# Kernel optimization log

Hardware: AMD Instinct MI355X
Metric: run time of the kernel (lower is better)

Reference implementation:

```python
import jax, jax.numpy as jnp
import numpy as np

EPS = 1e-6

def _rms_norm(x, w):
    # normalize over last dim (head_dim)
    var = jnp.mean(jnp.square(x), axis=-1, keepdims=True)
    return x * jax.lax.rsqrt(var + EPS) * w

def _rotate_half(x):
    half = x.shape[-1] // 2
    first, second = x[..., :half], x[..., half:]
    return jnp.concatenate([-second, first], axis=-1)

def _apply_rope(x, cos, sin):
    # x: [B,H,S,D]; cos/sin: [B,S,D] -> broadcast over heads
    return x * cos[:, None] + _rotate_half(x) * sin[:, None]

def setup_inputs() -> dict:
    key = jax.random.key(0)
    ks = jax.random.split(key, 10)
    B, Sq, Sk, Dm, H = 2, 2048, 2048, 2048, 16
    hd = Dm // H
    scale = 1.0 / np.sqrt(Dm)
    return {
        "x": jax.random.normal(ks[0], (B, Sq, Dm), jnp.float32),
        "context": jax.random.normal(ks[1], (B, Sk, Dm), jnp.float32),
        "cos_q": jax.random.uniform(ks[2], (B, Sq, hd), jnp.float32),
        "sin_q": jax.random.uniform(ks[3], (B, Sq, hd), jnp.float32),
        "cos_k": jax.random.uniform(ks[4], (B, Sk, hd), jnp.float32),
        "sin_k": jax.random.uniform(ks[5], (B, Sk, hd), jnp.float32),
        "Wq": jax.random.normal(ks[6], (Dm, Dm), jnp.float32) * scale,
        "Wk": jax.random.normal(ks[7], (Dm, Dm), jnp.float32) * scale,
        "Wv": jax.random.normal(ks[8], (Dm, Dm), jnp.float32) * scale,
        "Wo": jax.random.normal(ks[9], (Dm, Dm), jnp.float32) * scale,
        "q_norm_w": jnp.ones((hd,), jnp.float32),
        "k_norm_w": jnp.ones((hd,), jnp.float32),
    }

def reference(x, context, cos_q, sin_q, cos_k, sin_k, Wq, Wk, Wv, Wo, q_norm_w, k_norm_w):
    B, Sq, Dm = x.shape
    hd = q_norm_w.shape[0]
    H = Dm // hd
    # projections (torch Linear: y = x @ W.T), reshape to [B,H,S,D]
    q = (x @ Wq.T).reshape(B, Sq, H, hd).transpose(0, 2, 1, 3)
    k = (context @ Wk.T).reshape(B, -1, H, hd).transpose(0, 2, 1, 3)
    v = (context @ Wv.T).reshape(B, -1, H, hd).transpose(0, 2, 1, 3)
    # per-head QK RMSNorm
    q = _rms_norm(q, q_norm_w)
    k = _rms_norm(k, k_norm_w)
    # RoPE
    q = _apply_rope(q, cos_q, sin_q)
    k = _apply_rope(k, cos_k, sin_k)
    # SDPA, scale = 1/sqrt(head_dim)
    scale = 1.0 / np.sqrt(hd).astype(np.float32)
    scores = jnp.einsum('bhqd,bhkd->bhqk', q, k) * scale
    attn = jax.nn.softmax(scores, axis=-1)
    y = jnp.einsum('bhqk,bhkd->bhqd', attn, v)
    y = y.transpose(0, 2, 1, 3).reshape(B, Sq, Dm)
    return y @ Wo.T
```

## Files before the change

kernel.cpp:

```cpp
#include <hip/hip_runtime.h>


typedef __attribute__((ext_vector_type(8))) short bf16x8;
typedef __attribute__((ext_vector_type(4))) float f32x4;

#define AS1(p) ((__attribute__((address_space(1))) void*)(p))
#define AS3(p) ((__attribute__((address_space(3))) void*)(p))

__device__ __forceinline__ unsigned short f2bf(float f) {
  unsigned int u = __float_as_uint(f);
  u += 0x7fffu + ((u >> 16) & 1u);
  return (unsigned short)(u >> 16);
}
__device__ __forceinline__ float bf2f(unsigned short u) {
  return __uint_as_float(((unsigned int)u) << 16);
}

constexpr int B_ = 2, S_ = 2048, DM = 2048, H_ = 16, HD = 128;
constexpr int M_ = B_ * S_;

__global__ __launch_bounds__(256) void castbf(const float* __restrict__ X,
                                              unsigned short* __restrict__ Y, int n4) {
  int i = blockIdx.x * 256 + threadIdx.x;
  if (i >= n4) return;
  float4 v = ((const float4*)X)[i];
  ushort4 u;
  u.x = f2bf(v.x); u.y = f2bf(v.y); u.z = f2bf(v.z); u.w = f2bf(v.w);
  ((ushort4*)Y)[i] = u;
}

__global__ __launch_bounds__(256) void gemm_qkv(const unsigned short* __restrict__ xb,
                                                const unsigned short* __restrict__ cb,
                                                const unsigned short* __restrict__ Wq,
                                                const unsigned short* __restrict__ Wk,
                                                const unsigned short* __restrict__ Wv,
                                                unsigned short* __restrict__ Pq,
                                                unsigned short* __restrict__ Pk,
                                                unsigned short* __restrict__ Pv) {
  __shared__ unsigned short lA[128 * 32];
  __shared__ unsigned short lB[128 * 32];
  const int z = blockIdx.z;
  const unsigned short* A  = (z == 0) ? xb : cb;
  const unsigned short* Bw = (z == 0) ? Wq : (z == 1) ? Wk : Wv;
  unsigned short* C        = (z == 0) ? Pq : (z == 1) ? Pk : Pv;
  const int tid = threadIdx.x, wave = tid >> 6, lane = tid & 63;
  const int quad = lane >> 4, l16 = lane & 15;
  const int m0 = blockIdx.x * 128, n0 = blockIdx.y * 128;
  const int wm = (wave >> 1) * 64, wn = (wave & 1) * 64;
  f32x4 acc[4][4];
#pragma unroll
  for (int i = 0; i < 4; i++)
#pragma unroll
    for (int j = 0; j < 4; j++) acc[i][j] = (f32x4){0.f, 0.f, 0.f, 0.f};

  for (int k0 = 0; k0 < DM; k0 += 32) {
    __syncthreads();
#pragma unroll
    for (int call = 0; call < 2; ++call) {
      int c = wave * 128 + call * 64 + lane;
      int row = c >> 2, s = c & 3;
      int dc = s ^ ((row >> 1) & 3);
      __builtin_amdgcn_global_load_lds(AS1(A + (size_t)(m0 + row) * DM + k0 + dc * 8),
                                       AS3(lA + (wave * 128 + call * 64) * 8), 16, 0, 0);
      __builtin_amdgcn_global_load_lds(AS1(Bw + (size_t)(n0 + row) * DM + k0 + dc * 8),
                                       AS3(lB + (wave * 128 + call * 64) * 8), 16, 0, 0);
    }
    __syncthreads();

    bf16x8 af[4], bfr[4];
#pragma unroll
    for (int i = 0; i < 4; i++) {
      int r = wm + i * 16 + l16;
      af[i] = *(const bf16x8*)(lA + r * 32 + (quad ^ ((r >> 1) & 3)) * 8);
      int cN = wn + i * 16 + l16;
      bfr[i] = *(const bf16x8*)(lB + cN * 32 + (quad ^ ((cN >> 1) & 3)) * 8);
    }
#pragma unroll
    for (int i = 0; i < 4; i++)
#pragma unroll
      for (int j = 0; j < 4; j++)
        acc[i][j] = __builtin_amdgcn_mfma_f32_16x16x32_bf16(af[i], bfr[j], acc[i][j], 0, 0, 0);
  }
#pragma unroll
  for (int i = 0; i < 4; i++)
#pragma unroll
    for (int j = 0; j < 4; j++) {
      unsigned short* cp = C + (size_t)(m0 + wm + i * 16 + quad * 4) * DM + (n0 + wn + j * 16 + l16);
#pragma unroll
      for (int r = 0; r < 4; r++) cp[(size_t)r * DM] = f2bf(acc[i][j][r]);
    }
}

__global__ __launch_bounds__(256) void gemm_bt(const unsigned short* __restrict__ A,
                                               const unsigned short* __restrict__ Bw,
                                               float* __restrict__ C,
                                               int M, int N, int K) {
  __shared__ unsigned short lA[128 * 32];
  __shared__ unsigned short lB[128 * 32];
  const int tid = threadIdx.x, wave = tid >> 6, lane = tid & 63;
  const int quad = lane >> 4, l16 = lane & 15;
  const int m0 = blockIdx.x * 128, n0 = blockIdx.y * 128;
  const int wm = (wave >> 1) * 64, wn = (wave & 1) * 64;
  f32x4 acc[4][4];
#pragma unroll
  for (int i = 0; i < 4; i++)
#pragma unroll
    for (int j = 0; j < 4; j++) acc[i][j] = (f32x4){0.f, 0.f, 0.f, 0.f};

  for (int k0 = 0; k0 < K; k0 += 32) {
    __syncthreads();
#pragma unroll
    for (int call = 0; call < 2; ++call) {
      int c = wave * 128 + call * 64 + lane;
      int row = c >> 2, s = c & 3;
      int dc = s ^ ((row >> 1) & 3);
      __builtin_amdgcn_global_load_lds(AS1(A + (size_t)(m0 + row) * K + k0 + dc * 8),
                                       AS3(lA + (wave * 128 + call * 64) * 8), 16, 0, 0);
      __builtin_amdgcn_global_load_lds(AS1(Bw + (size_t)(n0 + row) * K + k0 + dc * 8),
                                       AS3(lB + (wave * 128 + call * 64) * 8), 16, 0, 0);
    }
    __syncthreads();

    bf16x8 af[4], bfr[4];
#pragma unroll
    for (int i = 0; i < 4; i++) {
      int r = wm + i * 16 + l16;
      af[i] = *(const bf16x8*)(lA + r * 32 + (quad ^ ((r >> 1) & 3)) * 8);
      int cN = wn + i * 16 + l16;
      bfr[i] = *(const bf16x8*)(lB + cN * 32 + (quad ^ ((cN >> 1) & 3)) * 8);
    }
#pragma unroll
    for (int i = 0; i < 4; i++)
#pragma unroll
      for (int j = 0; j < 4; j++)
        acc[i][j] = __builtin_amdgcn_mfma_f32_16x16x32_bf16(af[i], bfr[j], acc[i][j], 0, 0, 0);
  }
#pragma unroll
  for (int i = 0; i < 4; i++)
#pragma unroll
    for (int j = 0; j < 4; j++) {
      float* cp = C + (size_t)(m0 + wm + i * 16 + quad * 4) * N + (n0 + wn + j * 16 + l16);
#pragma unroll
      for (int r = 0; r < 4; r++) cp[(size_t)r * N] = acc[i][j][r];
    }
}

__global__ __launch_bounds__(256) void normrope(const unsigned short* __restrict__ X,
                                                const float* __restrict__ Cs,
                                                const float* __restrict__ Sn,
                                                const float* __restrict__ W,
                                                unsigned short* __restrict__ Out,
                                                float scale) {
  int gw = (blockIdx.x * 256 + threadIdx.x) >> 6;
  int lane = threadIdx.x & 63;
  int h = gw & 15, bs = gw >> 4;
  int s = bs & (S_ - 1), b = bs >> 11;
  const unsigned short* xr = X + (size_t)gw * HD;
  float x0 = bf2f(xr[lane]), x1 = bf2f(xr[lane + 64]);
  float ss = x0 * x0 + x1 * x1;
#pragma unroll
  for (int off = 32; off > 0; off >>= 1) ss += __shfl_xor(ss, off);
  float rr = rsqrtf(ss * (1.0f / 128.0f) + 1e-6f);
  float n0 = x0 * rr * W[lane], n1 = x1 * rr * W[lane + 64];
  const float* cp = Cs + (size_t)bs * HD;
  const float* sp = Sn + (size_t)bs * HD;
  float o0 = (n0 * cp[lane] - n1 * sp[lane]) * scale;
  float o1 = (n1 * cp[lane + 64] + n0 * sp[lane + 64]) * scale;
  unsigned short* orow = Out + (((size_t)(b * H_ + h)) * S_ + s) * HD;
  orow[lane] = f2bf(o0);
  orow[lane + 64] = f2bf(o1);
}

__global__ __launch_bounds__(256) void vtrans(const unsigned short* __restrict__ Vf,
                                              unsigned short* __restrict__ Vt) {
  __shared__ unsigned short tile[128 * 72];
  const int tid = threadIdx.x;
  const int sc = blockIdx.x & 31;
  const int bh = blockIdx.x >> 5;
  const int b = bh >> 4, h = bh & 15;
  const int s0 = sc * 64;
#pragma unroll
  for (int it = 0; it < 4; ++it) {
    int ci = it * 256 + tid;
    int s = ci >> 4, dc = ci & 15;
    bf16x8 v = *(const bf16x8*)(Vf + ((size_t)(b * S_ + s0 + s)) * DM + h * HD + dc * 8);
    unsigned short* tp = tile + (dc * 8) * 72 + s;
#pragma unroll
    for (int e = 0; e < 8; e++) tp[e * 72] = (unsigned short)v[e];
  }
  __syncthreads();
#pragma unroll
  for (int it = 0; it < 4; ++it) {
    int cj = it * 256 + tid;
    int d = cj >> 3, scx = cj & 7;
    bf16x8 vv = *(const bf16x8*)(tile + d * 72 + scx * 8);
    *(bf16x8*)(Vt + ((size_t)bh * HD + d) * S_ + s0 + scx * 8) = vv;
  }
}

__global__ __launch_bounds__(128) void flash(const unsigned short* __restrict__ Q,
                                             const unsigned short* __restrict__ Kt,
                                             const unsigned short* __restrict__ Vt,
                                             unsigned short* __restrict__ Y) {
  __shared__ unsigned short lK[64 * HD];
  __shared__ unsigned short lV[HD * 64];
  __shared__ unsigned short lP[2 * 1024];
  const int tid = threadIdx.x, wave = tid >> 6, lane = tid & 63;
  const int quad = lane >> 4, l16 = lane & 15;
  const int qb = blockIdx.x & 31;
  const int bh = blockIdx.x >> 5;
  const int b = bh >> 4, h = bh & 15;
  const int q0 = qb * 64 + wave * 32;

  bf16x8 aq[2][4];
#pragma unroll
  for (int u = 0; u < 2; u++) {
    const unsigned short* qrow = Q + ((size_t)bh * S_ + q0 + u * 16 + l16) * HD;
#pragma unroll
    for (int t = 0; t < 4; t++) aq[u][t] = *(const bf16x8*)(qrow + t * 32 + quad * 8);
  }
  f32x4 o[2][8];
#pragma unroll
  for (int u = 0; u < 2; u++)
#pragma unroll
    for (int t = 0; t < 8; t++) o[u][t] = (f32x4){0.f, 0.f, 0.f, 0.f};
  float lsum[2][4] = {{0.f, 0.f, 0.f, 0.f}, {0.f, 0.f, 0.f, 0.f}};

  const unsigned short* kbase = Kt + (size_t)bh * S_ * HD;
  const unsigned short* vbase = Vt + (size_t)bh * HD * S_;
  unsigned short* lPw = lP + wave * 1024;
  const int mrow = quad * 4;
  const int xsl = (l16 >> 1) & 3;
  const int xsl7 = (l16 >> 1) & 7;

  for (int k0 = 0; k0 < S_; k0 += 64) {
    __syncthreads();
#pragma unroll
    for (int call = 0; call < 8; ++call) {
      int c = call * 128 + wave * 64 + lane;
      int key = c >> 4, sk = c & 15;
      int dck = sk ^ (key & 15);
      __builtin_amdgcn_global_load_lds(AS1(kbase + (size_t)(k0 + key) * HD + dck * 8),
                                       AS3(lK + (call * 128 + wave * 64) * 8), 16, 0, 0);
      int dv = c >> 3, sv = c & 7;
      int kc = sv ^ ((dv >> 1) & 7);
      __builtin_amdgcn_global_load_lds(AS1(vbase + (size_t)dv * S_ + k0 + kc * 8),
                                       AS3(lV + (call * 128 + wave * 64) * 8), 16, 0, 0);
    }
    __syncthreads();

#pragma unroll
    for (int h2 = 0; h2 < 2; ++h2) {
      f32x4 s0[2] = {(f32x4){0.f, 0.f, 0.f, 0.f}, (f32x4){0.f, 0.f, 0.f, 0.f}};
      f32x4 s1[2] = {(f32x4){0.f, 0.f, 0.f, 0.f}, (f32x4){0.f, 0.f, 0.f, 0.f}};
      {
        const unsigned short* krow0 = lK + (h2 * 32 + l16) * HD;
        const unsigned short* krow1 = krow0 + 16 * HD;
#pragma unroll
        for (int t = 0; t < 4; t++) {
          int dcq = t * 4 + quad;
          bf16x8 kf0 = *(const bf16x8*)(krow0 + (dcq ^ l16) * 8);
          bf16x8 kf1 = *(const bf16x8*)(krow1 + (dcq ^ l16) * 8);
#pragma unroll
          for (int u = 0; u < 2; u++) {
            s0[u] = __builtin_amdgcn_mfma_f32_16x16x32_bf16(aq[u][t], kf0, s0[u], 0, 0, 0);
            s1[u] = __builtin_amdgcn_mfma_f32_16x16x32_bf16(aq[u][t], kf1, s1[u], 0, 0, 0);
          }
        }
      }
#pragma unroll
      for (int u = 0; u < 2; u++) {
        unsigned short* lPu = lPw + u * 512;
#pragma unroll
        for (int r = 0; r < 4; r++) {
          int m = mrow + r;
          int sx = (m >> 1) & 3;
          float p0 = __expf(s0[u][r]);
          float p1 = __expf(s1[u][r]);
          lsum[u][r] += p0 + p1;
          int kc0 = l16 >> 3;
          lPu[m * 32 + ((kc0 ^ sx)) * 8 + (l16 & 7)] = f2bf(p0);
          lPu[m * 32 + (((kc0 + 2) ^ sx)) * 8 + (l16 & 7)] = f2bf(p1);
        }
      }
      bf16x8 pf[2];
#pragma unroll
      for (int u = 0; u < 2; u++)
        pf[u] = *(const bf16x8*)(lPw + u * 512 + l16 * 32 + (quad ^ xsl) * 8);
#pragma unroll
      for (int t = 0; t < 8; t++) {
        bf16x8 vf = *(const bf16x8*)(lV + (t * 16 + l16) * 64 + ((h2 * 4 + quad) ^ xsl7) * 8);
#pragma unroll
        for (int u = 0; u < 2; u++)
          o[u][t] = __builtin_amdgcn_mfma_f32_16x16x32_bf16(pf[u], vf, o[u][t], 0, 0, 0);
      }
    }
  }

#pragma unroll
  for (int off = 1; off < 16; off <<= 1) {
#pragma unroll
    for (int u = 0; u < 2; u++)
#pragma unroll
      for (int r = 0; r < 4; r++) lsum[u][r] += __shfl_xor(lsum[u][r], off);
  }
  float inv[2][4];
#pragma unroll
  for (int u = 0; u < 2; u++)
#pragma unroll
    for (int r = 0; r < 4; r++) inv[u][r] = 1.0f / lsum[u][r];
#pragma unroll
  for (int u = 0; u < 2; u++)
#pragma unroll
    for (int t = 0; t < 8; t++)
#pragma unroll
      for (int r = 0; r < 4; r++) {
        size_t idx = ((size_t)b * S_ + q0 + u * 16 + mrow + r) * DM + h * HD + t * 16 + l16;
        Y[idx] = f2bf(o[u][t][r] * inv[u][r]);
      }
}

extern "C" void kernel_launch(void* const* d_in, const int* in_sizes, int n_in,
                              void* d_out, int out_size, void* d_ws, size_t ws_size,
                              hipStream_t stream) {
  const float* x    = (const float*)d_in[0];
  const float* ctx  = (const float*)d_in[1];
  const float* cosq = (const float*)d_in[2];
  const float* sinq = (const float*)d_in[3];
  const float* cosk = (const float*)d_in[4];
  const float* sink = (const float*)d_in[5];
  const float* Wq   = (const float*)d_in[6];
  const float* Wk   = (const float*)d_in[7];
  const float* Wv   = (const float*)d_in[8];
  const float* Wo   = (const float*)d_in[9];
  const float* qw   = (const float*)d_in[10];
  const float* kw   = (const float*)d_in[11];

  char* ws = (char*)d_ws;
  const size_t ACT2 = (size_t)M_ * DM * 2;
  const size_t W2   = (size_t)DM * DM * 2;
  unsigned short* xb  = (unsigned short*)(ws);
  unsigned short* cb  = (unsigned short*)(ws + ACT2);
  unsigned short* Wqb = (unsigned short*)(ws + 2 * ACT2);
  unsigned short* Wkb = (unsigned short*)(ws + 2 * ACT2 + W2);
  unsigned short* Wvb = (unsigned short*)(ws + 2 * ACT2 + 2 * W2);
  unsigned short* Wob = (unsigned short*)(ws + 2 * ACT2 + 3 * W2);
  unsigned short* Pq  = (unsigned short*)(ws + 2 * ACT2 + 4 * W2);
  unsigned short* Pk  = (unsigned short*)(ws + 3 * ACT2 + 4 * W2);
  unsigned short* Pv  = (unsigned short*)(ws + 4 * ACT2 + 4 * W2);
  unsigned short* qn = xb;
  unsigned short* kn = Wqb;
  unsigned short* vt = cb;
  unsigned short* yb = Pq;

  const float scale = 0.0883883476483184f;

  castbf<<<M_ * DM / 1024, 256, 0, stream>>>(x, xb, M_ * DM / 4);
  castbf<<<M_ * DM / 1024, 256, 0, stream>>>(ctx, cb, M_ * DM / 4);
  castbf<<<DM * DM / 1024, 256, 0, stream>>>(Wq, Wqb, DM * DM / 4);
  castbf<<<DM * DM / 1024, 256, 0, stream>>>(Wk, Wkb, DM * DM / 4);
  castbf<<<DM * DM / 1024, 256, 0, stream>>>(Wv, Wvb, DM * DM / 4);
  castbf<<<DM * DM / 1024, 256, 0, stream>>>(Wo, Wob, DM * DM / 4);

  dim3 gq(M_ / 128, DM / 128, 3);
  gemm_qkv<<<gq, 256, 0, stream>>>(xb, cb, Wqb, Wkb, Wvb, Pq, Pk, Pv);

  normrope<<<M_ * H_ / 4, 256, 0, stream>>>(Pq, cosq, sinq, qw, qn, scale);
  normrope<<<M_ * H_ / 4, 256, 0, stream>>>(Pk, cosk, sink, kw, kn, 1.0f);
  vtrans<<<B_ * H_ * (S_ / 64), 256, 0, stream>>>(Pv, vt);

  flash<<<B_ * H_ * (S_ / 64), 128, 0, stream>>>(qn, kn, vt, yb);

  dim3 gg(M_ / 128, DM / 128);
  gemm_bt<<<gg, 256, 0, stream>>>(yb, Wob, (float*)d_out, M_, DM, DM);

  (void)in_sizes; (void)n_in; (void)out_size; (void)ws_size;
}
```

Measured before the change: 499.2 us.

## Pipeline GEMMs with 4-stage LDS ring, 256x128 tiles, and MFMA priority boosts

```diff
diff --git a/kernel.cpp b/kernel.cpp
--- a/kernel.cpp
+++ b/kernel.cpp
@@ -29,120 +29,113 @@
   ((ushort4*)Y)[i] = u;
 }
 
-__global__ __launch_bounds__(256) void gemm_qkv(const unsigned short* __restrict__ xb,
-                                                const unsigned short* __restrict__ cb,
-                                                const unsigned short* __restrict__ Wq,
-                                                const unsigned short* __restrict__ Wk,
-                                                const unsigned short* __restrict__ Wv,
-                                                unsigned short* __restrict__ Pq,
-                                                unsigned short* __restrict__ Pk,
-                                                unsigned short* __restrict__ Pv) {
-  __shared__ unsigned short lA[128 * 32];
-  __shared__ unsigned short lB[128 * 32];
+template <int BF16OUT>
+__device__ __forceinline__ void gemm_core(const unsigned short* __restrict__ A,
+                                          const unsigned short* __restrict__ Bw,
+                                          void* __restrict__ Cv,
+                                          unsigned short* lA, unsigned short* lB) {
+  const int tid = threadIdx.x, wave = tid >> 6, lane = tid & 63;
+  const int quad = lane >> 4, l16 = lane & 15;
+  const int m0 = blockIdx.x * 256, n0 = blockIdx.y * 128;
+  const int wm = (wave >> 1) * 64, wn = (wave & 1) * 64;
+  constexpr int NT = DM / 32;
+
+  f32x4 acc[4][4];
+#pragma unroll
+  for (int i = 0; i < 4; i++)
+#pragma unroll
+    for (int j = 0; j < 4; j++) acc[i][j] = (f32x4){0.f, 0.f, 0.f, 0.f};
+
+  const int c0 = wave * 64 + lane;
+  const int rA0 = c0 >> 2, dA0 = (c0 & 3) ^ ((rA0 >> 1) & 3);
+  const int c1 = 512 + c0;
+  const int rA1 = c1 >> 2, dA1 = (c1 & 3) ^ ((rA1 >> 1) & 3);
+  const unsigned short* gA0 = A + (size_t)(m0 + rA0) * DM + dA0 * 8;
+  const unsigned short* gA1 = A + (size_t)(m0 + rA1) * DM + dA1 * 8;
+  const unsigned short* gB  = Bw + (size_t)(n0 + rA0) * DM + dA0 * 8;
+  const int wdst = wave * 512;
+
+#define STAGE(T)                                                                         \
+  {                                                                                      \
+    const int b_ = (T) & 3; const int k_ = (T) << 5;                                     \
+    __builtin_amdgcn_global_load_lds(AS1(gA0 + k_), AS3(lA + b_ * 8192 + wdst), 16, 0, 0);\
+    __builtin_amdgcn_global_load_lds(AS1(gA1 + k_), AS3(lA + b_ * 8192 + 4096 + wdst), 16, 0, 0);\
+    __builtin_amdgcn_global_load_lds(AS1(gB + k_),  AS3(lB + b_ * 4096 + wdst), 16, 0, 0);\
+  }
+
+  STAGE(0) STAGE(1) STAGE(2)
+
+  const int xoff = (quad ^ ((l16 >> 1) & 3)) * 8;
+
+  for (int t = 0; t < NT; ++t) {
+    if (t < NT - 2)       asm volatile("s_waitcnt vmcnt(6)\n\ts_barrier" ::: "memory");
+    else if (t == NT - 2) asm volatile("s_waitcnt vmcnt(3)\n\ts_barrier" ::: "memory");
+    else                  asm volatile("s_waitcnt vmcnt(0)\n\ts_barrier" ::: "memory");
+
+    const unsigned short* ab = lA + (t & 3) * 8192;
+    const unsigned short* bb = lB + (t & 3) * 4096;
+    bf16x8 af[4], bf[4];
+#pragma unroll
+    for (int i = 0; i < 4; i++)
+      af[i] = *(const bf16x8*)(ab + (wm + i * 16 + l16) * 32 + xoff);
+#pragma unroll
+    for (int j = 0; j < 4; j++)
+      bf[j] = *(const bf16x8*)(bb + (wn + j * 16 + l16) * 32 + xoff);
+
+    if (t + 3 < NT) STAGE(t + 3)
+
+    __builtin_amdgcn_s_barrier();
+    __builtin_amdgcn_s_setprio(1);
+#pragma unroll
+    for (int i = 0; i < 4; i++)
+#pragma unroll
+      for (int j = 0; j < 4; j++)
+        acc[i][j] = __builtin_amdgcn_mfma_f32_16x16x32_bf16(af[i], bf[j], acc[i][j], 0, 0, 0);
+    __builtin_amdgcn_s_setprio(0);
+  }
+#undef STAGE
+
+#pragma unroll
+  for (int i = 0; i < 4; i++)
+#pragma unroll
+    for (int j = 0; j < 4; j++) {
+      const size_t row = (size_t)(m0 + wm + i * 16 + quad * 4);
+      const int col = n0 + wn + j * 16 + l16;
+      if (BF16OUT) {
+        unsigned short* cp = (unsigned short*)Cv + row * DM + col;
+#pragma unroll
+        for (int r = 0; r < 4; r++) cp[(size_t)r * DM] = f2bf(acc[i][j][r]);
+      } else {
+        float* cp = (float*)Cv + row * DM + col;
+#pragma unroll
+        for (int r = 0; r < 4; r++) cp[(size_t)r * DM] = acc[i][j][r];
+      }
+    }
+}
+
+__global__ __launch_bounds__(512, 2) void gemm_qkv(const unsigned short* __restrict__ xb,
+                                                   const unsigned short* __restrict__ cb,
+                                                   const unsigned short* __restrict__ Wq,
+                                                   const unsigned short* __restrict__ Wk,
+                                                   const unsigned short* __restrict__ Wv,
+                                                   unsigned short* __restrict__ Pq,
+                                                   unsigned short* __restrict__ Pk,
+                                                   unsigned short* __restrict__ Pv) {
+  __shared__ __align__(16) unsigned short lA[4 * 8192];
+  __shared__ __align__(16) unsigned short lB[4 * 4096];
   const int z = blockIdx.z;
   const unsigned short* A  = (z == 0) ? xb : cb;
   const unsigned short* Bw = (z == 0) ? Wq : (z == 1) ? Wk : Wv;
   unsigned short* C        = (z == 0) ? Pq : (z == 1) ? Pk : Pv;
-  const int tid = threadIdx.x, wave = tid >> 6, lane = tid & 63;
-  const int quad = lane >> 4, l16 = lane & 15;
-  const int m0 = blockIdx.x * 128, n0 = blockIdx.y * 128;
-  const int wm = (wave >> 1) * 64, wn = (wave & 1) * 64;
-  f32x4 acc[4][4];
-#pragma unroll
-  for (int i = 0; i < 4; i++)
-#pragma unroll
-    for (int j = 0; j < 4; j++) acc[i][j] = (f32x4){0.f, 0.f, 0.f, 0.f};
-
-  for (int k0 = 0; k0 < DM; k0 += 32) {
-    __syncthreads();
-#pragma unroll
-    for (int call = 0; call < 2; ++call) {
-      int c = wave * 128 + call * 64 + lane;
-      int row = c >> 2, s = c & 3;
-      int dc = s ^ ((row >> 1) & 3);
-      __builtin_amdgcn_global_load_lds(AS1(A + (size_t)(m0 + row) * DM + k0 + dc * 8),
-                                       AS3(lA + (wave * 128 + call * 64) * 8), 16, 0, 0);
-      __builtin_amdgcn_global_load_lds(AS1(Bw + (size_t)(n0 + row) * DM + k0 + dc * 8),
-                                       AS3(lB + (wave * 128 + call * 64) * 8), 16, 0, 0);
-    }
-    __syncthreads();
-
-    bf16x8 af[4], bfr[4];
-#pragma unroll
-    for (int i = 0; i < 4; i++) {
-      int r = wm + i * 16 + l16;
-      af[i] = *(const bf16x8*)(lA + r * 32 + (quad ^ ((r >> 1) & 3)) * 8);
-      int cN = wn + i * 16 + l16;
-      bfr[i] = *(const bf16x8*)(lB + cN * 32 + (quad ^ ((cN >> 1) & 3)) * 8);
-    }
-#pragma unroll
-    for (int i = 0; i < 4; i++)
-#pragma unroll
-      for (int j = 0; j < 4; j++)
-        acc[i][j] = __builtin_amdgcn_mfma_f32_16x16x32_bf16(af[i], bfr[j], acc[i][j], 0, 0, 0);
-  }
-#pragma unroll
-  for (int i = 0; i < 4; i++)
-#pragma unroll
-    for (int j = 0; j < 4; j++) {
-      unsigned short* cp = C + (size_t)(m0 + wm + i * 16 + quad * 4) * DM + (n0 + wn + j * 16 + l16);
-#pragma unroll
-      for (int r = 0; r < 4; r++) cp[(size_t)r * DM] = f2bf(acc[i][j][r]);
-    }
-}
-
-__global__ __launch_bounds__(256) void gemm_bt(const unsigned short* __restrict__ A,
-                                               const unsigned short* __restrict__ Bw,
-                                               float* __restrict__ C,
-                                               int M, int N, int K) {
-  __shared__ unsigned short lA[128 * 32];
-  __shared__ unsigned short lB[128 * 32];
-  const int tid = threadIdx.x, wave = tid >> 6, lane = tid & 63;
-  const int quad = lane >> 4, l16 = lane & 15;
-  const int m0 = blockIdx.x * 128, n0 = blockIdx.y * 128;
-  const int wm = (wave >> 1) * 64, wn = (wave & 1) * 64;
-  f32x4 acc[4][4];
-#pragma unroll
-  for (int i = 0; i < 4; i++)
-#pragma unroll
-    for (int j = 0; j < 4; j++) acc[i][j] = (f32x4){0.f, 0.f, 0.f, 0.f};
-
-  for (int k0 = 0; k0 < K; k0 += 32) {
-    __syncthreads();
-#pragma unroll
-    for (int call = 0; call < 2; ++call) {
-      int c = wave * 128 + call * 64 + lane;
-      int row = c >> 2, s = c & 3;
-      int dc = s ^ ((row >> 1) & 3);
-      __builtin_amdgcn_global_load_lds(AS1(A + (size_t)(m0 + row) * K + k0 + dc * 8),
-                                       AS3(lA + (wave * 128 + call * 64) * 8), 16, 0, 0);
-      __builtin_amdgcn_global_load_lds(AS1(Bw + (size_t)(n0 + row) * K + k0 + dc * 8),
-                                       AS3(lB + (wave * 128 + call * 64) * 8), 16, 0, 0);
-    }
-    __syncthreads();
-
-    bf16x8 af[4], bfr[4];
-#pragma unroll
-    for (int i = 0; i < 4; i++) {
-      int r = wm + i * 16 + l16;
-      af[i] = *(const bf16x8*)(lA + r * 32 + (quad ^ ((r >> 1) & 3)) * 8);
-      int cN = wn + i * 16 + l16;
-      bfr[i] = *(const bf16x8*)(lB + cN * 32 + (quad ^ ((cN >> 1) & 3)) * 8);
-    }
-#pragma unroll
-    for (int i = 0; i < 4; i++)
-#pragma unroll
-      for (int j = 0; j < 4; j++)
-        acc[i][j] = __builtin_amdgcn_mfma_f32_16x16x32_bf16(af[i], bfr[j], acc[i][j], 0, 0, 0);
-  }
-#pragma unroll
-  for (int i = 0; i < 4; i++)
-#pragma unroll
-    for (int j = 0; j < 4; j++) {
-      float* cp = C + (size_t)(m0 + wm + i * 16 + quad * 4) * N + (n0 + wn + j * 16 + l16);
-#pragma unroll
-      for (int r = 0; r < 4; r++) cp[(size_t)r * N] = acc[i][j][r];
-    }
+  gemm_core<1>(A, Bw, C, lA, lB);
+}
+
+__global__ __launch_bounds__(512, 2) void gemm_bt(const unsigned short* __restrict__ A,
+                                                  const unsigned short* __restrict__ Bw,
+                                                  float* __restrict__ C) {
+  __shared__ __align__(16) unsigned short lA[4 * 8192];
+  __shared__ __align__(16) unsigned short lB[4 * 4096];
+  gemm_core<0>(A, Bw, C, lA, lB);
 }
 
 __global__ __launch_bounds__(256) void normrope(const unsigned short* __restrict__ X,
@@ -256,6 +249,7 @@
       {
         const unsigned short* krow0 = lK + (h2 * 32 + l16) * HD;
         const unsigned short* krow1 = krow0 + 16 * HD;
+        __builtin_amdgcn_s_setprio(1);
 #pragma unroll
         for (int t = 0; t < 4; t++) {
           int dcq = t * 4 + quad;
@@ -267,6 +261,7 @@
             s1[u] = __builtin_amdgcn_mfma_f32_16x16x32_bf16(aq[u][t], kf1, s1[u], 0, 0, 0);
           }
         }
+        __builtin_amdgcn_s_setprio(0);
       }
 #pragma unroll
       for (int u = 0; u < 2; u++) {
@@ -287,6 +282,7 @@
 #pragma unroll
       for (int u = 0; u < 2; u++)
         pf[u] = *(const bf16x8*)(lPw + u * 512 + l16 * 32 + (quad ^ xsl) * 8);
+      __builtin_amdgcn_s_setprio(1);
 #pragma unroll
       for (int t = 0; t < 8; t++) {
         bf16x8 vf = *(const bf16x8*)(lV + (t * 16 + l16) * 64 + ((h2 * 4 + quad) ^ xsl7) * 8);
@@ -294,6 +290,7 @@
         for (int u = 0; u < 2; u++)
           o[u][t] = __builtin_amdgcn_mfma_f32_16x16x32_bf16(pf[u], vf, o[u][t], 0, 0, 0);
       }
+      __builtin_amdgcn_s_setprio(0);
     }
   }
 
@@ -362,8 +359,8 @@
   castbf<<<DM * DM / 1024, 256, 0, stream>>>(Wv, Wvb, DM * DM / 4);
   castbf<<<DM * DM / 1024, 256, 0, stream>>>(Wo, Wob, DM * DM / 4);
 
-  dim3 gq(M_ / 128, DM / 128, 3);
-  gemm_qkv<<<gq, 256, 0, stream>>>(xb, cb, Wqb, Wkb, Wvb, Pq, Pk, Pv);
+  dim3 gq(M_ / 256, DM / 128, 3);
+  gemm_qkv<<<gq, 512, 0, stream>>>(xb, cb, Wqb, Wkb, Wvb, Pq, Pk, Pv);
 
   normrope<<<M_ * H_ / 4, 256, 0, stream>>>(Pq, cosq, sinq, qw, qn, scale);
   normrope<<<M_ * H_ / 4, 256, 0, stream>>>(Pk, cosk, sink, kw, kn, 1.0f);
@@ -371,8 +368,8 @@
 
   flash<<<B_ * H_ * (S_ / 64), 128, 0, stream>>>(qn, kn, vt, yb);
 
-  dim3 gg(M_ / 128, DM / 128);
-  gemm_bt<<<gg, 256, 0, stream>>>(yb, Wob, (float*)d_out, M_, DM, DM);
+  dim3 gg(M_ / 256, DM / 128);
+  gemm_bt<<<gg, 512, 0, stream>>>(yb, Wob, (float*)d_out);
 
   (void)in_sizes; (void)n_in; (void)out_size; (void)ws_size;
 }
```

Result: faster. 489.3 us (-2.0%).
